# Kernel tuning notes

Hardware: AMD Instinct MI355X
Metric: run time of the kernel (lower is better)

## Reference

```python
import jax, jax.numpy as jnp
import numpy as np

B, S, D, H, I = 4, 1024, 2048, 16, 8192
HD = D // H
S_IMG = 576
EPS = 1e-5


def _layer_norm(x, w, b):
    mu = jnp.mean(x, axis=-1, keepdims=True)
    var = jnp.var(x, axis=-1, keepdims=True)
    return (x - mu) * jax.lax.rsqrt(var + EPS) * w + b


def setup_inputs() -> dict:
    key = jax.random.key(0)
    ks = jax.random.split(key, 12)
    s = 0.02
    return {
        "image_features": jax.random.normal(ks[0], (B, S_IMG, D), jnp.float32),
        "hidden_states": jax.random.normal(ks[1], (B, S, D), jnp.float32),
        "attention_mask": jnp.ones((B, S), jnp.float32),
        "causal_attention_mask": jnp.zeros((B, 1, S, S), jnp.float32),
        "Wq": jax.random.normal(ks[2], (D, D), jnp.float32) * s,
        "bq": jnp.zeros((D,), jnp.float32),
        "Wk": jax.random.normal(ks[3], (D, D), jnp.float32) * s,
        "bk": jnp.zeros((D,), jnp.float32),
        "Wv": jax.random.normal(ks[4], (D, D), jnp.float32) * s,
        "bv": jnp.zeros((D,), jnp.float32),
        "Wo": jax.random.normal(ks[5], (D, D), jnp.float32) * s,
        "bo": jnp.zeros((D,), jnp.float32),
        "ln1_w": jnp.ones((D,), jnp.float32),
        "ln1_b": jnp.zeros((D,), jnp.float32),
        "ln2_w": jnp.ones((D,), jnp.float32),
        "ln2_b": jnp.zeros((D,), jnp.float32),
        "W1": jax.random.normal(ks[6], (I, D), jnp.float32) * s,
        "b1": jnp.zeros((I,), jnp.float32),
        "W2": jax.random.normal(ks[7], (D, I), jnp.float32) * s,
        "b2": jnp.zeros((D,), jnp.float32),
    }


def reference(image_features, hidden_states, attention_mask, causal_attention_mask,
              Wq, bq, Wk, bk, Wv, bv, Wo, bo,
              ln1_w, ln1_b, ln2_w, ln2_b, W1, b1, W2, b2):
    dtype = hidden_states.dtype
    scale = HD ** (-0.5)
    # expand_mask: [B,S] -> additive mask [B,1,S,S]
    inverted = 1.0 - attention_mask[:, None, None, :].astype(dtype)  # [B,1,1,S]
    add_mask = jnp.where(inverted.astype(bool), jnp.finfo(dtype).min, inverted)
    add_mask = jnp.broadcast_to(add_mask, (B, 1, S, S))

    residual = hidden_states
    x = _layer_norm(hidden_states, ln1_w, ln1_b)

    q = (x @ Wq.T + bq) * scale
    k = x @ Wk.T + bk
    v = x @ Wv.T + bv
    q = q.reshape(B, S, H, HD)
    k = k.reshape(B, S, H, HD)
    v = v.reshape(B, S, H, HD)

    scores = jnp.einsum('bqhd,bkhd->bhqk', q, k) + add_mask  # [B,H,S,S]
    probs = jax.nn.softmax(scores, axis=-1)
    attn = jnp.einsum('bhqk,bkhd->bqhd', probs, v).reshape(B, S, D)
    attn = attn @ Wo.T + bo

    hidden = residual + attn
    residual = hidden
    y = _layer_norm(hidden, ln2_w, ln2_b)
    y = jax.nn.gelu(y @ W1.T + b1, approximate=False)
    y = y @ W2.T + b2
    return residual + y
```

## Files before the change

### kernel.cpp

```cpp
#include <hip/hip_runtime.h>
#include <hip/hip_bf16.h>
#include <math.h>

typedef __hip_bfloat16 bf16;
typedef __attribute__((ext_vector_type(8))) short short8;
typedef __attribute__((ext_vector_type(4))) float floatx4;

constexpr int Bc = 4, Sc = 1024, Dc = 2048, Hc = 16, HDc = 128, Ic = 8192;
constexpr int QKVLD = 3 * Dc;

__device__ __forceinline__ float bf2f(bf16 x){ return __bfloat162float(x); }
__device__ __forceinline__ bf16 f2bf(float x){ return __float2bfloat16(x); }

__device__ __forceinline__ uint4 pack8(float4 a, float4 b){
    union { uint4 u; bf16 h[8]; } r;
    r.h[0]=f2bf(a.x); r.h[1]=f2bf(a.y); r.h[2]=f2bf(a.z); r.h[3]=f2bf(a.w);
    r.h[4]=f2bf(b.x); r.h[5]=f2bf(b.y); r.h[6]=f2bf(b.z); r.h[7]=f2bf(b.w);
    return r.u;
}

__device__ __forceinline__ void glds16(void* lds, const void* g){
    __builtin_amdgcn_global_load_lds(
        (__attribute__((address_space(1))) void*)(size_t)g,
        (__attribute__((address_space(3))) void*)lds,
        16, 0, 0);
}

__global__ __launch_bounds__(256)
void conv_w(const float* __restrict__ src, bf16* __restrict__ dst){
    const size_t i = ((size_t)blockIdx.x * 256 + threadIdx.x) * 8;
    float4 a = *(const float4*)(src + i);
    float4 b = *(const float4*)(src + i + 4);
    *(uint4*)(dst + i) = pack8(a, b);
}

__global__ __launch_bounds__(256)
void conv_w4(const float* __restrict__ s0, const float* __restrict__ s1,
             const float* __restrict__ s2, const float* __restrict__ s3,
             bf16* __restrict__ dst){
    const int id = blockIdx.x >> 11;
    const float* src = (id == 0) ? s0 : (id == 1) ? s1 : (id == 2) ? s2 : s3;
    const size_t i = ((size_t)(blockIdx.x & 2047) * 256 + threadIdx.x) * 8;
    float4 a = *(const float4*)(src + i);
    float4 b = *(const float4*)(src + i + 4);
    *(uint4*)(dst + (size_t)id * Dc * Dc + i) = pack8(a, b);
}

__global__ __launch_bounds__(256)
void init_add(float* __restrict__ dst, const float* __restrict__ bias,
              const float* __restrict__ src){
    const size_t i = ((size_t)blockIdx.x * 256 + threadIdx.x) * 8;
    const int col = (int)(i & (Dc - 1));
    float4 a = *(const float4*)(src + i);
    float4 b = *(const float4*)(src + i + 4);
    float4 ba = *(const float4*)(bias + col);
    float4 bb = *(const float4*)(bias + col + 4);
    a.x += ba.x; a.y += ba.y; a.z += ba.z; a.w += ba.w;
    b.x += bb.x; b.y += bb.y; b.z += bb.z; b.w += bb.w;
    *(float4*)(dst + i) = a;
    *(float4*)(dst + i + 4) = b;
}

template<int INF32>
__global__ __launch_bounds__(256)
void ln_kernel(const void* __restrict__ x, const float* __restrict__ w,
               const float* __restrict__ b, bf16* __restrict__ y)
{
    const int row = blockIdx.x;
    const int t = threadIdx.x;
    float f[8], s = 0.f, s2 = 0.f;
    if (INF32) {
        const float* xr = (const float*)x + (size_t)row * Dc + t * 8;
        float4 a = *(const float4*)xr, c = *(const float4*)(xr + 4);
        f[0]=a.x; f[1]=a.y; f[2]=a.z; f[3]=a.w; f[4]=c.x; f[5]=c.y; f[6]=c.z; f[7]=c.w;
    } else {
        union { uint4 u; bf16 h[8]; } ld;
        ld.u = *(const uint4*)((const bf16*)x + (size_t)row * Dc + t * 8);
#pragma unroll
        for (int j = 0; j < 8; ++j) f[j] = bf2f(ld.h[j]);
    }
#pragma unroll
    for (int j = 0; j < 8; ++j) { s += f[j]; s2 += f[j] * f[j]; }
#pragma unroll
    for (int off = 32; off; off >>= 1) { s += __shfl_xor(s, off); s2 += __shfl_xor(s2, off); }
    __shared__ float red[8];
    const int wave = t >> 6, lane = t & 63;
    if (lane == 0) { red[wave] = s; red[4 + wave] = s2; }
    __syncthreads();
    s  = red[0] + red[1] + red[2] + red[3];
    s2 = red[4] + red[5] + red[6] + red[7];
    const float mean = s * (1.0f / Dc);
    const float var  = s2 * (1.0f / Dc) - mean * mean;
    const float rs   = rsqrtf(var + 1e-5f);
    union { uint4 u; bf16 h[8]; } st;
#pragma unroll
    for (int j = 0; j < 8; ++j) {
        const int col = t * 8 + j;
        st.h[j] = f2bf((f[j] - mean) * rs * w[col] + b[col]);
    }
    *(uint4*)&y[(size_t)row * Dc + t * 8] = st.u;
}

template<int EPI, int RESF32, int OUTF32>
__global__ __launch_bounds__(256)
void gemm_bt(const bf16* __restrict__ A, const bf16* __restrict__ W,
             const float* __restrict__ bias, const float* __restrict__ bias2,
             const float* __restrict__ bias3, const void* __restrict__ res,
             void* __restrict__ C, int M, int N, int K, float scale)
{
    __shared__ __align__(16) bf16 As[128 * 64];
    __shared__ __align__(16) bf16 Bs[128 * 64];
    const int tile_m = blockIdx.y * 128;
    const int tile_n = blockIdx.x * 128;
    const int t = threadIdx.x;
    const int wave = t >> 6, lane = t & 63, quad = lane >> 4, l16 = lane & 15;
    const int wm = (wave >> 1) * 64, wn = (wave & 1) * 64;
    const int Klen = K / gridDim.z, kbeg = blockIdx.z * Klen;

    floatx4 acc[4][4] = {};

    const int r8 = t >> 3, c8 = t & 7;
    const int cg = (c8 - r8) & 7;
    const bf16* Ab = A + (size_t)(tile_m + r8) * K + kbeg + cg * 8;
    const bf16* Wb = W + (size_t)(tile_n + r8) * K + kbeg + cg * 8;
    char* AsB = (char*)As;
    char* BsB = (char*)Bs;
    const int wb = wave * 1024;

    for (int k0 = 0; k0 < Klen; k0 += 64) {
        __syncthreads();
#pragma unroll
        for (int u = 0; u < 4; ++u) {
            glds16(AsB + u * 4096 + wb, Ab + (size_t)(u * 32) * K + k0);
            glds16(BsB + u * 4096 + wb, Wb + (size_t)(u * 32) * K + k0);
        }
        __syncthreads();
#pragma unroll
        for (int ks = 0; ks < 2; ++ks) {
            short8 af[4], bfr[4];
#pragma unroll
            for (int mi = 0; mi < 4; ++mi)
                af[mi] = *(const short8*)&As[(wm + mi * 16 + l16) * 64 + ((ks * 4 + quad + l16) & 7) * 8];
#pragma unroll
            for (int ni = 0; ni < 4; ++ni)
                bfr[ni] = *(const short8*)&Bs[(wn + ni * 16 + l16) * 64 + ((ks * 4 + quad + l16) & 7) * 8];
#pragma unroll
            for (int mi = 0; mi < 4; ++mi)
#pragma unroll
                for (int ni = 0; ni < 4; ++ni)
                    acc[mi][ni] = __builtin_amdgcn_mfma_f32_16x16x32_bf16(af[mi], bfr[ni], acc[mi][ni], 0, 0, 0);
        }
    }

#pragma unroll
    for (int mi = 0; mi < 4; ++mi) {
        const int row0 = tile_m + wm + mi * 16 + quad * 4;
#pragma unroll
        for (int ni = 0; ni < 4; ++ni) {
            const int col = tile_n + wn + ni * 16 + l16;
            float bv = 0.f, sc = 1.f;
            if (EPI == 4) {
                if (col < 2048)      { bv = bias[col];         sc = scale; }
                else if (col < 4096) { bv = bias2[col - 2048]; }
                else                 { bv = bias3[col - 4096]; }
            } else if (EPI != 5) {
                bv = bias[col];
            }
#pragma unroll
            for (int r = 0; r < 4; ++r) {
                const size_t idx = (size_t)(row0 + r) * N + col;
                float v = acc[mi][ni][r];
                if (EPI == 5) { atomicAdd(&((float*)C)[idx], v); continue; }
                v += bv;
                if (EPI == 1) v *= scale;
                if (EPI == 4) v *= sc;
                if (EPI == 2) v = 0.5f * v * (1.0f + erff(v * 0.70710678118f));
                if (EPI == 3) v += RESF32 ? ((const float*)res)[idx] : bf2f(((const bf16*)res)[idx]);
                if (OUTF32) ((float*)C)[idx] = v;
                else        ((bf16*)C)[idx] = f2bf(v);
            }
        }
    }
}

__global__ __launch_bounds__(256)
void flash_attn(const bf16* __restrict__ QKV, const float* __restrict__ mask,
                bf16* __restrict__ O)
{
    __shared__ __align__(16) bf16 Ks[4 * 64 * 32];
    __shared__ __align__(16) bf16 Vt[128 * 72];
    __shared__ __align__(16) bf16 Ps[4][16 * 72];
    const int bh = blockIdx.y, b = bh >> 4, h = bh & 15;
    const int t = threadIdx.x, w = t >> 6, lane = t & 63, quad = lane >> 4, l16 = lane & 15;
    const int qbase = blockIdx.x * 64 + w * 16;
    const size_t rowb = (size_t)b * Sc;
    const bf16* Kp = QKV + 2048 + (size_t)h * HDc;
    const bf16* Vp = QKV + 4096 + (size_t)h * HDc;

    short8 qf[4];
    {
        const bf16* qp = QKV + (rowb + qbase + l16) * QKVLD + (size_t)h * HDc + quad * 8;
#pragma unroll
        for (int kc = 0; kc < 4; ++kc) qf[kc] = *(const short8*)(qp + kc * 32);
    }
    float m_i[4], l_i[4];
    floatx4 Oacc[8] = {};
#pragma unroll
    for (int r = 0; r < 4; ++r) { m_i[r] = -1e30f; l_i[r] = 0.f; }

    const int p2 = t & 31, dg = t >> 5;

    for (int kt = 0; kt < Sc; kt += 64) {
        __syncthreads();
#pragma unroll
        for (int u = 0; u < 4; ++u) {
            const int row = u * 16 + (lane >> 2);
            glds16((char*)Ks + w * 4096 + u * 1024,
                   Kp + (rowb + kt + row) * QKVLD + w * 32 + (lane & 3) * 8);
        }
        {
            union { uint4 u4; unsigned short s[8]; } va[2][2];
#pragma unroll
            for (int kk = 0; kk < 2; ++kk) {
                const bf16* vp = Vp + (rowb + kt + 2 * p2 + kk) * QKVLD + dg * 16;
                va[kk][0].u4 = *(const uint4*)vp;
                va[kk][1].u4 = *(const uint4*)(vp + 8);
            }
            unsigned* VtW = (unsigned*)Vt;
#pragma unroll
            for (int j = 0; j < 16; ++j) {
                const unsigned word = (unsigned)va[0][j >> 3].s[j & 7]
                                    | ((unsigned)va[1][j >> 3].s[j & 7] << 16);
                VtW[(dg * 16 + j) * 36 + p2] = word;
            }
        }
        __syncthreads();

        floatx4 sacc[4] = {};
#pragma unroll
        for (int kc = 0; kc < 4; ++kc)
#pragma unroll
            for (int sub = 0; sub < 4; ++sub) {
                short8 kf = *(const short8*)&Ks[kc * 2048 + (sub * 16 + l16) * 32 + quad * 8];
                sacc[sub] = __builtin_amdgcn_mfma_f32_16x16x32_bf16(qf[kc], kf, sacc[sub], 0, 0, 0);
            }
#pragma unroll
        for (int sub = 0; sub < 4; ++sub) {
            const float mv = mask[b * Sc + kt + sub * 16 + l16];
            const float madd = (mv < 0.5f) ? -3.0e38f : 0.f;
#pragma unroll
            for (int r = 0; r < 4; ++r) sacc[sub][r] += madd;
        }
        float p[4][4], alpha[4];
#pragma unroll
        for (int r = 0; r < 4; ++r) {
            float mx = fmaxf(fmaxf(sacc[0][r], sacc[1][r]), fmaxf(sacc[2][r], sacc[3][r]));
#pragma unroll
            for (int off = 8; off; off >>= 1) mx = fmaxf(mx, __shfl_xor(mx, off));
            const float mnew = fmaxf(m_i[r], mx);
            alpha[r] = exp2f(m_i[r] - mnew);
            float ps = 0.f;
#pragma unroll
            for (int sub = 0; sub < 4; ++sub) { p[sub][r] = exp2f(sacc[sub][r] - mnew); ps += p[sub][r]; }
#pragma unroll
            for (int off = 8; off; off >>= 1) ps += __shfl_xor(ps, off);
            l_i[r] = l_i[r] * alpha[r] + ps;
            m_i[r] = mnew;
        }
#pragma unroll
        for (int nsub = 0; nsub < 8; ++nsub)
#pragma unroll
            for (int r = 0; r < 4; ++r) Oacc[nsub][r] *= alpha[r];

        bf16* Pw = Ps[w];
#pragma unroll
        for (int sub = 0; sub < 4; ++sub)
#pragma unroll
            for (int r = 0; r < 4; ++r)
                Pw[(quad * 4 + r) * 72 + sub * 16 + l16] = f2bf(p[sub][r]);
        const short8 pf0 = *(const short8*)&Pw[l16 * 72 + quad * 8];
        const short8 pf1 = *(const short8*)&Pw[l16 * 72 + 32 + quad * 8];
#pragma unroll
        for (int nsub = 0; nsub < 8; ++nsub) {
            const short8 vf0 = *(const short8*)&Vt[(nsub * 16 + l16) * 72 + quad * 8];
            const short8 vf1 = *(const short8*)&Vt[(nsub * 16 + l16) * 72 + 32 + quad * 8];
            Oacc[nsub] = __builtin_amdgcn_mfma_f32_16x16x32_bf16(pf0, vf0, Oacc[nsub], 0, 0, 0);
            Oacc[nsub] = __builtin_amdgcn_mfma_f32_16x16x32_bf16(pf1, vf1, Oacc[nsub], 0, 0, 0);
        }
    }

#pragma unroll
    for (int r = 0; r < 4; ++r) {
        const float inv = 1.f / l_i[r];
        bf16* orow = O + (rowb + qbase + quad * 4 + r) * Dc + (size_t)h * HDc;
#pragma unroll
        for (int nsub = 0; nsub < 8; ++nsub)
            orow[nsub * 16 + l16] = f2bf(Oacc[nsub][r] * inv);
    }
}

extern "C" void kernel_launch(void* const* d_in, const int* in_sizes, int n_in,
                              void* d_out, int out_size, void* d_ws, size_t ws_size,
                              hipStream_t stream)
{
    const float* hidden = (const float*)d_in[1];
    const float* amask  = (const float*)d_in[2];
    const float* Wq = (const float*)d_in[4];  const float* bq = (const float*)d_in[5];
    const float* Wk = (const float*)d_in[6];  const float* bk = (const float*)d_in[7];
    const float* Wv = (const float*)d_in[8];  const float* bv = (const float*)d_in[9];
    const float* Wo = (const float*)d_in[10]; const float* bo = (const float*)d_in[11];
    const float* ln1w = (const float*)d_in[12]; const float* ln1b = (const float*)d_in[13];
    const float* ln2w = (const float*)d_in[14]; const float* ln2b = (const float*)d_in[15];
    const float* W1 = (const float*)d_in[16]; const float* b1 = (const float*)d_in[17];
    const float* W2 = (const float*)d_in[18]; const float* b2 = (const float*)d_in[19];

    const size_t UE = 8ull * 1024 * 1024;
    const size_t WE = 4ull * 1024 * 1024;
    bf16*  U = (bf16*)d_ws;
    bf16*  qkv   = U;
    bf16*  wbuf  = U + 4 * UE;
    bf16*  x_ln  = U + 6 * UE;
    float* hid2f = (float*)(U + 6 * UE);
    bf16*  ffn1  = U;
    bf16*  attn  = (bf16*)d_out;
    bf16*  y_ln  = (bf16*)d_out + UE;
    float* outf  = (float*)d_out;

    const float qscale = 0.08838834764831845f * 1.4426950408889634f;
    const dim3 gQKV(QKVLD / 128, Bc * Sc / 128, 1);
    const dim3 gSK (Dc / 128,    Bc * Sc / 128, 2);
    const dim3 gF1 (Ic / 128,    Bc * Sc / 128, 1);

    conv_w4<<<8192, 256, 0, stream>>>(Wq, Wk, Wv, Wo, wbuf);
    ln_kernel<1><<<Bc * Sc, 256, 0, stream>>>(hidden, ln1w, ln1b, x_ln);
    gemm_bt<4,0,0><<<gQKV, 256, 0, stream>>>(x_ln, wbuf, bq, bk, bv, nullptr, qkv,
                                             Bc * Sc, QKVLD, Dc, qscale);
    flash_attn<<<dim3(Sc / 64, Bc * Hc), 256, 0, stream>>>(qkv, amask, attn);
    init_add<<<4096, 256, 0, stream>>>(hid2f, bo, hidden);
    gemm_bt<5,0,1><<<gSK, 256, 0, stream>>>(attn, wbuf + 3 * WE, nullptr, nullptr, nullptr,
                                            nullptr, hid2f, Bc * Sc, Dc, Dc, 0.f);
    ln_kernel<1><<<Bc * Sc, 256, 0, stream>>>(hid2f, ln2w, ln2b, y_ln);
    conv_w<<<8192, 256, 0, stream>>>(W1, wbuf);
    gemm_bt<2,0,0><<<gF1, 256, 0, stream>>>(y_ln, wbuf, b1, nullptr, nullptr, nullptr, ffn1,
                                            Bc * Sc, Ic, Dc, 0.f);
    init_add<<<4096, 256, 0, stream>>>(outf, b2, hid2f);
    conv_w<<<8192, 256, 0, stream>>>(W2, wbuf);
    gemm_bt<5,0,1><<<gSK, 256, 0, stream>>>(ffn1, wbuf, nullptr, nullptr, nullptr,
                                            nullptr, outf, Bc * Sc, Dc, Ic, 0.f);
}
```

Measured before the change: 982.2 us.

## Rewrite GEMM as 256x256 tile, 8-wave double-buffered pipelined kernel with swizzled block order

The GEMM kernel moves from 128x128 tiles with 4 waves and a single-buffered load/sync loop to 256x256 tiles with 8 waves. It uses 128KB of double-buffered LDS and interleaves async global-to-LDS staging of the next K tile with MFMA phases, using explicit barriers, waitcnts and setprio. Block IDs are remapped in groups of eight, likely for cache locality. The aim is to hide memory latency and raise data reuse per tile. The cost is heavier register and LDS use, occupancy limited to one block per CU, and fewer blocks for the smaller GEMMs.

```diff
diff --git a/kernel.cpp b/kernel.cpp
--- a/kernel.cpp
+++ b/kernel.cpp
@@ -101,63 +101,134 @@
     *(uint4*)&y[(size_t)row * Dc + t * 8] = st.u;
 }
 
+
+#define BAR()   __builtin_amdgcn_s_barrier()
+#define LGKM0() asm volatile("s_waitcnt lgkmcnt(0)" ::: "memory")
+#define VMW2()  asm volatile("s_waitcnt vmcnt(2)" ::: "memory")
+#define VMW0()  asm volatile("s_waitcnt vmcnt(0)" ::: "memory")
+#define SCB0()  __builtin_amdgcn_sched_barrier(0)
+#define PRIO(x) __builtin_amdgcn_s_setprio(x)
+
 template<int EPI, int RESF32, int OUTF32>
-__global__ __launch_bounds__(256)
+__global__ __launch_bounds__(512, 2)
 void gemm_bt(const bf16* __restrict__ A, const bf16* __restrict__ W,
              const float* __restrict__ bias, const float* __restrict__ bias2,
              const float* __restrict__ bias3, const void* __restrict__ res,
              void* __restrict__ C, int M, int N, int K, float scale)
 {
-    __shared__ __align__(16) bf16 As[128 * 64];
-    __shared__ __align__(16) bf16 Bs[128 * 64];
-    const int tile_m = blockIdx.y * 128;
-    const int tile_n = blockIdx.x * 128;
+    __shared__ __align__(16) char lds[131072];
+
+    const int nwgx = gridDim.x;
+    const int nwg  = nwgx * gridDim.y;
+    int bid = blockIdx.y * nwgx + blockIdx.x;
+    bid = (bid & 7) * (nwg >> 3) + (bid >> 3);
+    const int tile_n = (bid % nwgx) * 256;
+    const int tile_m = (bid / nwgx) * 256;
+
     const int t = threadIdx.x;
     const int wave = t >> 6, lane = t & 63, quad = lane >> 4, l16 = lane & 15;
-    const int wm = (wave >> 1) * 64, wn = (wave & 1) * 64;
+    const int wmp = wave >> 2, wnp = wave & 3;
     const int Klen = K / gridDim.z, kbeg = blockIdx.z * Klen;
-
-    floatx4 acc[4][4] = {};
-
-    const int r8 = t >> 3, c8 = t & 7;
-    const int cg = (c8 - r8) & 7;
-    const bf16* Ab = A + (size_t)(tile_m + r8) * K + kbeg + cg * 8;
-    const bf16* Wb = W + (size_t)(tile_n + r8) * K + kbeg + cg * 8;
-    char* AsB = (char*)As;
-    char* BsB = (char*)Bs;
-    const int wb = wave * 1024;
-
-    for (int k0 = 0; k0 < Klen; k0 += 64) {
-        __syncthreads();
-#pragma unroll
-        for (int u = 0; u < 4; ++u) {
-            glds16(AsB + u * 4096 + wb, Ab + (size_t)(u * 32) * K + k0);
-            glds16(BsB + u * 4096 + wb, Wb + (size_t)(u * 32) * K + k0);
-        }
-        __syncthreads();
-#pragma unroll
-        for (int ks = 0; ks < 2; ++ks) {
-            short8 af[4], bfr[4];
-#pragma unroll
-            for (int mi = 0; mi < 4; ++mi)
-                af[mi] = *(const short8*)&As[(wm + mi * 16 + l16) * 64 + ((ks * 4 + quad + l16) & 7) * 8];
-#pragma unroll
-            for (int ni = 0; ni < 4; ++ni)
-                bfr[ni] = *(const short8*)&Bs[(wn + ni * 16 + l16) * 64 + ((ks * 4 + quad + l16) & 7) * 8];
-#pragma unroll
-            for (int mi = 0; mi < 4; ++mi)
-#pragma unroll
-                for (int ni = 0; ni < 4; ++ni)
-                    acc[mi][ni] = __builtin_amdgcn_mfma_f32_16x16x32_bf16(af[mi], bfr[ni], acc[mi][ni], 0, 0, 0);
-        }
-    }
-
-#pragma unroll
-    for (int mi = 0; mi < 4; ++mi) {
-        const int row0 = tile_m + wm + mi * 16 + quad * 4;
+    const int NT = Klen >> 6;
+
+    const int g8  = lane & 7;
+    const int lr0 = wave * 16 + (lane >> 3);
+    const int lr1 = lr0 + 8;
+    const int c0 = (g8 - lr0) & 7, c1 = (g8 - lr1) & 7;
+    const size_t aof0 = (size_t)(tile_m + (lr0 >> 6) * 128 + (lr0 & 63)) * K + kbeg + c0 * 8;
+    const size_t aof1 = (size_t)(tile_m + (lr1 >> 6) * 128 + (lr1 & 63)) * K + kbeg + c1 * 8;
+    const size_t bof0 = (size_t)(tile_n + lr0) * K + kbeg + c0 * 8;
+    const size_t bof1 = (size_t)(tile_n + lr1) * K + kbeg + c1 * 8;
+    const int ls0 = wave * 2048, ls1 = wave * 2048 + 1024;
+
+    const int ard = (wmp * 64 + l16) * 128;
+    const int brd = 32768 + (wnp * 64 + l16) * 128;
+    const int gq0 = ((quad + l16) & 7) * 16;
+
+    floatx4 acc[8][4] = {};
+    short8 av[4], bv0[4], bv1[4];
+
+#define STAGE_A(_b, _mh, _kt) do { \
+    glds16(lds + (_b) * 65536 + (_mh) * 16384 + ls0, \
+           A + aof0 + (size_t)((_mh) * 64) * K + (_kt) * 64); \
+    glds16(lds + (_b) * 65536 + (_mh) * 16384 + ls1, \
+           A + aof1 + (size_t)((_mh) * 64) * K + (_kt) * 64); \
+} while (0)
+
+#define STAGE_B(_b, _h, _kt) do { \
+    glds16(lds + (_b) * 65536 + 32768 + (_h) * 16384 + ls0, \
+           W + bof0 + (size_t)((_h) * 128) * K + (_kt) * 64); \
+    glds16(lds + (_b) * 65536 + 32768 + (_h) * 16384 + ls1, \
+           W + bof1 + (size_t)((_h) * 128) * K + (_kt) * 64); \
+} while (0)
+
+#define LDA4(_b, _mh, _ks) do { \
+    const char* _p = lds + (_b) * 65536 + (_mh) * 16384 + ard + (gq0 ^ ((_ks) * 64)); \
+    av[0] = *(const short8*)(_p);        av[1] = *(const short8*)(_p + 2048); \
+    av[2] = *(const short8*)(_p + 4096); av[3] = *(const short8*)(_p + 6144); \
+} while (0)
+
+#define LDB4(_b, _ks, _arr) do { \
+    const char* _p = lds + (_b) * 65536 + brd + (gq0 ^ ((_ks) * 64)); \
+    _arr[0] = *(const short8*)(_p);        _arr[1] = *(const short8*)(_p + 2048); \
+    _arr[2] = *(const short8*)(_p + 4096); _arr[3] = *(const short8*)(_p + 6144); \
+} while (0)
+
+#define MFB(_mh, _bv) do { \
+    _Pragma("unroll") \
+    for (int _mi = 0; _mi < 4; ++_mi) { \
+        _Pragma("unroll") \
+        for (int _ni = 0; _ni < 4; ++_ni) \
+            acc[(_mh) * 4 + _mi][_ni] = __builtin_amdgcn_mfma_f32_16x16x32_bf16( \
+                av[_mi], _bv[_ni], acc[(_mh) * 4 + _mi][_ni], 0, 0, 0); \
+    } \
+} while (0)
+
+#define TILE(_bb, _tt) do { \
+     \
+    LDA4(_bb, 0, 0); LDB4(_bb, 0, bv0); \
+    if ((_tt) + 1 < NT) { STAGE_A((_bb) ^ 1, 1, (_tt) + 1); STAGE_B((_bb) ^ 1, 0, (_tt) + 1); } \
+    BAR(); LGKM0(); SCB0(); PRIO(1); MFB(0, bv0); PRIO(0); BAR(); \
+     \
+    LDA4(_bb, 0, 1); LDB4(_bb, 1, bv1); \
+    if ((_tt) + 1 < NT) STAGE_B((_bb) ^ 1, 1, (_tt) + 1); \
+    BAR(); LGKM0(); SCB0(); PRIO(1); MFB(0, bv1); PRIO(0); BAR(); \
+     \
+    LDA4(_bb, 1, 0); \
+    if ((_tt) + 2 < NT) STAGE_A(_bb, 0, (_tt) + 2); \
+    BAR(); LGKM0(); SCB0(); PRIO(1); MFB(1, bv0); PRIO(0); BAR(); \
+     \
+    LDA4(_bb, 1, 1); \
+    BAR(); LGKM0(); SCB0(); PRIO(1); MFB(1, bv1); PRIO(0); \
+    if ((_tt) + 2 < NT)      { VMW2(); } \
+    else if ((_tt) + 1 < NT) { VMW0(); } \
+    BAR(); \
+} while (0)
+
+    STAGE_A(0, 0, 0); STAGE_A(0, 1, 0);
+    STAGE_B(0, 0, 0); STAGE_B(0, 1, 0);
+    STAGE_A(1, 0, 1);
+    VMW2();
+    BAR();
+
+    for (int tt = 0; tt < NT; tt += 2) {
+        TILE(0, tt);
+        TILE(1, tt + 1);
+    }
+
+#undef TILE
+#undef MFB
+#undef LDB4
+#undef LDA4
+#undef STAGE_B
+#undef STAGE_A
+
+#pragma unroll
+    for (int mi = 0; mi < 8; ++mi) {
+        const int row0 = tile_m + wmp * 128 + mi * 16 + quad * 4;
 #pragma unroll
         for (int ni = 0; ni < 4; ++ni) {
-            const int col = tile_n + wn + ni * 16 + l16;
+            const int col = tile_n + wnp * 64 + ni * 16 + l16;
             float bv = 0.f, sc = 1.f;
             if (EPI == 4) {
                 if (col < 2048)      { bv = bias[col];         sc = scale; }
@@ -327,24 +398,25 @@
     float* outf  = (float*)d_out;
 
     const float qscale = 0.08838834764831845f * 1.4426950408889634f;
-    const dim3 gQKV(QKVLD / 128, Bc * Sc / 128, 1);
-    const dim3 gSK (Dc / 128,    Bc * Sc / 128, 2);
-    const dim3 gF1 (Ic / 128,    Bc * Sc / 128, 1);
+    const dim3 gQKV(QKVLD / 256, Bc * Sc / 256, 1);
+    const dim3 gWo (Dc / 256,    Bc * Sc / 256, 2);
+    const dim3 gF1 (Ic / 256,    Bc * Sc / 256, 1);
+    const dim3 gF2 (Dc / 256,    Bc * Sc / 256, 2);
 
     conv_w4<<<8192, 256, 0, stream>>>(Wq, Wk, Wv, Wo, wbuf);
     ln_kernel<1><<<Bc * Sc, 256, 0, stream>>>(hidden, ln1w, ln1b, x_ln);
-    gemm_bt<4,0,0><<<gQKV, 256, 0, stream>>>(x_ln, wbuf, bq, bk, bv, nullptr, qkv,
+    gemm_bt<4,0,0><<<gQKV, 512, 0, stream>>>(x_ln, wbuf, bq, bk, bv, nullptr, qkv,
                                              Bc * Sc, QKVLD, Dc, qscale);
     flash_attn<<<dim3(Sc / 64, Bc * Hc), 256, 0, stream>>>(qkv, amask, attn);
     init_add<<<4096, 256, 0, stream>>>(hid2f, bo, hidden);
-    gemm_bt<5,0,1><<<gSK, 256, 0, stream>>>(attn, wbuf + 3 * WE, nullptr, nullptr, nullptr,
+    gemm_bt<5,0,1><<<gWo, 512, 0, stream>>>(attn, wbuf + 3 * WE, nullptr, nullptr, nullptr,
                                             nullptr, hid2f, Bc * Sc, Dc, Dc, 0.f);
     ln_kernel<1><<<Bc * Sc, 256, 0, stream>>>(hid2f, ln2w, ln2b, y_ln);
     conv_w<<<8192, 256, 0, stream>>>(W1, wbuf);
-    gemm_bt<2,0,0><<<gF1, 256, 0, stream>>>(y_ln, wbuf, b1, nullptr, nullptr, nullptr, ffn1,
+    gemm_bt<2,0,0><<<gF1, 512, 0, stream>>>(y_ln, wbuf, b1, nullptr, nullptr, nullptr, ffn1,
                                             Bc * Sc, Ic, Dc, 0.f);
     init_add<<<4096, 256, 0, stream>>>(outf, b2, hid2f);
     conv_w<<<8192, 256, 0, stream>>>(W2, wbuf);
-    gemm_bt<5,0,1><<<gSK, 256, 0, stream>>>(ffn1, wbuf, nullptr, nullptr, nullptr,
+    gemm_bt<5,0,1><<<gF2, 512, 0, stream>>>(ffn1, wbuf, nullptr, nullptr, nullptr,
                                             nullptr, outf, Bc * Sc, Dc, Ic, 0.f);
 }
```

Result: faster. 950.4 us (-3.2%).
